# Optimization experiments

Measured on AMD Instinct MI355X. Metric: run time of the kernel, lower is better.

Reference implementation:

```python
import jax, jax.numpy as jnp
import numpy as np

H = 128  # hidden_dim


def _lstm_dir(x, w_ih, w_hh, b, reverse):
    """Single-direction LSTM over x:[B,T,I]. PyTorch gate order (i,f,g,o)."""
    B = x.shape[0]
    gx = jnp.einsum('bti,gi->btg', x, w_ih) + b        # [B,T,4H] input-side gates, one batched GEMM
    gx = jnp.swapaxes(gx, 0, 1)                        # [T,B,4H]
    if reverse:
        gx = gx[::-1]

    def step(carry, g_x):
        h, c = carry
        g = g_x + h @ w_hh.T                           # [B,4H]
        i, f, gg, o = jnp.split(g, 4, axis=-1)
        i = jax.nn.sigmoid(i)
        f = jax.nn.sigmoid(f)
        gg = jnp.tanh(gg)
        o = jax.nn.sigmoid(o)
        c = f * c + i * gg
        h = o * jnp.tanh(c)
        return (h, c), h

    init = (jnp.zeros((B, H), x.dtype), jnp.zeros((B, H), x.dtype))
    (hT, cT), hs = jax.lax.scan(step, init, gx)        # hs:[T,B,H]
    hs = jnp.swapaxes(hs, 0, 1)                        # [B,T,H]
    if reverse:
        hs = hs[:, ::-1]
    return hs, hT, cT


def _bilstm_layer(x, pf, pb):
    hf, hTf, cTf = _lstm_dir(x, *pf, reverse=False)
    hb, hTb, cTb = _lstm_dir(x, *pb, reverse=True)
    return jnp.concatenate([hf, hb], axis=-1), (hTf, cTf), (hTb, cTb)


def setup_inputs() -> dict:
    key = jax.random.key(0)
    ks = jax.random.split(key, 13)
    s = 1.0 / np.sqrt(H)
    B, T, I = 256, 512, 24
    d = {"x": jax.random.normal(ks[0], (B, T, I), jnp.float32)}
    # layer 0 input dim = 24; layer 1 input dim = 2*H = 256
    dims = {"l0f": I, "l0b": I, "l1f": 2 * H, "l1b": 2 * H}
    i = 1
    for tag, din in dims.items():
        d[f"w_ih_{tag}"] = jax.random.uniform(ks[i], (4 * H, din), jnp.float32, -s, s); i += 1
        d[f"w_hh_{tag}"] = jax.random.uniform(ks[i], (4 * H, H), jnp.float32, -s, s); i += 1
        d[f"b_{tag}"] = jax.random.uniform(ks[i], (4 * H,), jnp.float32, -s, s); i += 1
    return d


def reference(x,
              w_ih_l0f, w_hh_l0f, b_l0f, w_ih_l0b, w_hh_l0b, b_l0b,
              w_ih_l1f, w_hh_l1f, b_l1f, w_ih_l1b, w_hh_l1b, b_l1b):
    # Layer 0 (bidirectional)
    y0, (hTf0, cTf0), (hTb0, cTb0) = _bilstm_layer(
        x, (w_ih_l0f, w_hh_l0f, b_l0f), (w_ih_l0b, w_hh_l0b, b_l0b))
    # Inter-layer dropout is identity in eval mode.
    # Layer 1 (bidirectional)
    y1, (hTf1, cTf1), (hTb1, cTb1) = _bilstm_layer(
        y0, (w_ih_l1f, w_hh_l1f, b_l1f), (w_ih_l1b, w_hh_l1b, b_l1b))
    # PyTorch h_n/c_n layout: [num_layers*num_dirs, B, H] ordered l0f,l0b,l1f,l1b
    h_n = jnp.stack([hTf0, hTb0, hTf1, hTb1], axis=0)
    c_n = jnp.stack([cTf0, cTb0, cTf1, cTb1], axis=0)
    return y1, h_n, c_n
```

## Files before the change

kernel.cpp:

```cpp
#include <hip/hip_runtime.h>
#include <hip/hip_bf16.h>
#include <stdint.h>

#define Bn 256
#define Tn 512
#define Hn 128
#define G4 512
#define Mn (Bn*Tn)

typedef __attribute__((ext_vector_type(8))) short s16x8;
typedef __attribute__((ext_vector_type(4))) float f32x4;

__device__ __forceinline__ float b2f(unsigned short u) {
    union { unsigned int i; float f; } v; v.i = ((unsigned int)u) << 16; return v.f;
}
__device__ __forceinline__ unsigned short f2b(float f) {
    union { float f; unsigned int i; } v; v.f = f;
    unsigned int x = v.i;
    unsigned int r = (x + 0x7FFFu + ((x >> 16) & 1u)) >> 16;
    return (unsigned short)r;
}
__device__ __forceinline__ unsigned int pk2(float a, float b) {
    __hip_bfloat162 t = __float22bfloat162_rn(make_float2(a, b));
    union { __hip_bfloat162 v; unsigned int u; } c; c.v = t; return c.u;
}
__device__ __forceinline__ s16x8 cvt8v(const float* p) {
    f32x4 a = *(const f32x4*)p;
    f32x4 b = *(const f32x4*)(p + 4);
    s16x8 r;
    r[0] = (short)f2b(a[0]); r[1] = (short)f2b(a[1]);
    r[2] = (short)f2b(a[2]); r[3] = (short)f2b(a[3]);
    r[4] = (short)f2b(b[0]); r[5] = (short)f2b(b[1]);
    r[6] = (short)f2b(b[2]); r[7] = (short)f2b(b[3]);
    return r;
}
__device__ __forceinline__ float sigm(float x) {
    return __builtin_amdgcn_rcpf(1.f + __expf(-x));
}
__device__ __forceinline__ float tanh_f(float x) {
    return 1.f - 2.f * __builtin_amdgcn_rcpf(1.f + __expf(2.f * x));
}
__device__ __forceinline__ void gload16(const void* gsrc, void* lds) {
    __builtin_amdgcn_global_load_lds(
        (const __attribute__((address_space(1))) unsigned int*)gsrc,
        (__attribute__((address_space(3))) unsigned int*)lds, 16, 0, 0);
}
__device__ __forceinline__ void ldsbar() {
    asm volatile("s_waitcnt lgkmcnt(0)\n\ts_barrier" ::: "memory");
}

__global__ __launch_bounds__(256)
void prep(const float* __restrict__ x,
          const float* __restrict__ w0f, const float* __restrict__ w0b,
          const float* __restrict__ w1f, const float* __restrict__ w1b,
          unsigned short* __restrict__ xb,
          unsigned short* __restrict__ w0bf,
          unsigned short* __restrict__ w1bf)
{
    int tid = blockIdx.x * 256 + threadIdx.x;
    int nthr = gridDim.x * 256;
    for (int idx = tid; idx < Mn * 32; idx += nthr) {
        int row = idx >> 5, col = idx & 31;
        xb[idx] = f2b(col < 24 ? x[row * 24 + col] : 0.f);
    }
    for (int idx = tid; idx < 2 * 512 * 32; idx += nthr) {
        int d = idx >> 14, rem = idx & 16383;
        int n = rem >> 5, col = rem & 31;
        const float* w = d ? w0b : w0f;
        w0bf[idx] = f2b(col < 24 ? w[n * 24 + col] : 0.f);
    }
    for (int idx = tid; idx < 2 * 512 * 256; idx += nthr) {
        int d = idx >> 17, rem = idx & 131071;
        const float* w = d ? w1b : w1f;
        w1bf[idx] = f2b(w[rem]);
    }
}

template<int BK, int KOUT>
__global__ __launch_bounds__(256, 2)
void gemm_tile(const unsigned short* __restrict__ A, int lda,
               const unsigned short* __restrict__ W,
               unsigned short* __restrict__ gx)
{
    constexpr int GR = BK / 8;
    constexpr int SWM = (GR >= 8) ? 7 : (GR - 1);
    constexpr int ASZ = 128 * BK * 2;
    constexpr int GOFF = (BK == 128) ? 0 : 2 * ASZ;
    constexpr int SMEM = 2 * ASZ + ((BK == 128) ? 0 : 4 * 16 * 68 * 4);
    __shared__ char smem[SMEM];
    unsigned short* Atile = (unsigned short*)smem;
    unsigned short* Btile = (unsigned short*)(smem + ASZ);

    const int K = BK * KOUT;
    const int mb = blockIdx.x;
    const int nb = blockIdx.y;
    const int dir = nb >> 2, ncol0 = (nb & 3) * 128;
    const int row0 = mb * 128;
    const unsigned short* Asrc = A + (size_t)row0 * lda;
    const unsigned short* Bsrc = W + (size_t)dir * 512 * K + (size_t)ncol0 * K;
    unsigned short* out = gx + (size_t)dir * Mn * G4;

    const int tid = threadIdx.x;
    const int w = tid >> 6, l = tid & 63;
    const int q = l >> 4, i = l & 15;
    const int wm = w >> 1, wn = w & 1;

    f32x4 acc[4][4];
#pragma unroll
    for (int a = 0; a < 4; ++a)
#pragma unroll
        for (int b = 0; b < 4; ++b) acc[a][b] = f32x4{0.f, 0.f, 0.f, 0.f};

    for (int ko = 0; ko < KOUT; ++ko) {
#pragma unroll
        for (int it = 0; it < (128 * GR) / 256; ++it) {
            int g = it * 256 + tid;
            int row = g / GR, p = g % GR;
            int gi = p ^ (row & SWM);
            gload16(Asrc + (size_t)row * lda + ko * BK + gi * 8,
                    (char*)Atile + g * 16);
        }
#pragma unroll
        for (int it = 0; it < (128 * GR) / 256; ++it) {
            int g = it * 256 + tid;
            int row = g / GR, p = g % GR;
            int gi = p ^ (row & SWM);
            gload16(Bsrc + (size_t)row * K + ko * BK + gi * 8,
                    (char*)Btile + g * 16);
        }
        __syncthreads();
#pragma unroll
        for (int kf = 0; kf < BK / 32; ++kf) {
            s16x8 af[4], bf[4];
#pragma unroll
            for (int mt = 0; mt < 4; ++mt) {
                int ar = wm * 64 + mt * 16 + i;
                int p = (kf * 4 + q) ^ (ar & SWM);
                af[mt] = *(const s16x8*)((char*)Atile + (ar * GR + p) * 16);
            }
#pragma unroll
            for (int nt = 0; nt < 4; ++nt) {
                int br = wn * 64 + nt * 16 + i;
                int p = (kf * 4 + q) ^ (br & SWM);
                bf[nt] = *(const s16x8*)((char*)Btile + (br * GR + p) * 16);
            }
#pragma unroll
            for (int mt = 0; mt < 4; ++mt)
#pragma unroll
                for (int nt = 0; nt < 4; ++nt)
                    acc[mt][nt] = __builtin_amdgcn_mfma_f32_16x16x32_bf16(
                        af[mt], bf[nt], acc[mt][nt], 0, 0, 0);
        }
        __syncthreads();
    }

    float* gbufw = (float*)(smem + GOFF) + w * (16 * 68);
#pragma unroll
    for (int mt = 0; mt < 4; ++mt) {
#pragma unroll
        for (int nt = 0; nt < 4; ++nt)
#pragma unroll
            for (int r = 0; r < 4; ++r)
                gbufw[(q * 4 + r) * 68 + nt * 16 + i] = acc[mt][nt][r];
        __syncthreads();
#pragma unroll
        for (int it2 = 0; it2 < 2; ++it2) {
            int rr = (l >> 3) + it2 * 8;
            int cc = (l & 7) * 8;
            const float* gsrc = gbufw + rr * 68 + cc;
            uint4 pv;
            pv.x = pk2(gsrc[0], gsrc[1]);
            pv.y = pk2(gsrc[2], gsrc[3]);
            pv.z = pk2(gsrc[4], gsrc[5]);
            pv.w = pk2(gsrc[6], gsrc[7]);
            *(uint4*)(out + (size_t)(row0 + wm * 64 + mt * 16 + rr) * G4
                          + ncol0 + wn * 64 + cc) = pv;
        }
        __syncthreads();
    }
}

__global__ __launch_bounds__(256, 1)
void lstm_rec(const unsigned short* __restrict__ gx,
              const float* __restrict__ Whf,
              const float* __restrict__ Whb,
              const float* __restrict__ biasf,
              const float* __restrict__ biasb,
              float* __restrict__ y,
              unsigned short* __restrict__ y0b,
              float* __restrict__ hn,
              float* __restrict__ cn,
              int layer)
{
    const int b0  = blockIdx.x * 2;
    const int dir = blockIdx.y;
    const float* Wh   = dir ? Whb : Whf;
    const float* bias = dir ? biasb : biasf;
    const unsigned short* gxd = gx + (size_t)dir * Mn * G4;

    const int tid = threadIdx.x;
    const int w = tid >> 6, l = tid & 63;
    const int q = l >> 4, i = l & 15;

    __shared__ unsigned short hbuf[16][136];
    __shared__ float Gs[512][2];

    for (int idx = tid; idx < 16 * 136; idx += 256)
        ((unsigned short*)hbuf)[idx] = 0;

    s16x8 wh[8][4];
#pragma unroll
    for (int nt = 0; nt < 8; ++nt) {
        int n = w * 128 + nt * 16 + i;
#pragma unroll
        for (int kf = 0; kf < 4; ++kf)
            wh[nt][kf] = cvt8v(Wh + (size_t)n * Hn + kf * 32 + q * 8);
    }

    const int m = tid >> 7;
    const int j = tid & 127;
    const int b = b0 + m;
    const float bi = bias[j],       bf = bias[128 + j];
    const float bg = bias[256 + j], bo = bias[384 + j];
    float c = 0.f, hlast = 0.f;

    unsigned short bufA[4][8], bufB[4][8];
#pragma unroll
    for (int f = 0; f < 8; ++f) {
        int t = dir ? (Tn - 1 - f) : f;
        const unsigned short* gp = gxd + ((size_t)b * Tn + t) * G4;
        bufA[0][f] = gp[j];
        bufA[1][f] = gp[128 + j];
        bufA[2][f] = gp[256 + j];
        bufA[3][f] = gp[384 + j];
    }

    __syncthreads();

    auto do8 = [&](unsigned short (&useB)[4][8], unsigned short (&ldB)[4][8],
                   int sb) {
#pragma unroll
        for (int f = 0; f < 8; ++f) {
            const int s = sb + f;
            const int t = dir ? (Tn - 1 - s) : s;

            s16x8 ah[4];
#pragma unroll
            for (int kf = 0; kf < 4; ++kf)
                ah[kf] = *(const s16x8*)(&hbuf[i][kf * 32 + q * 8]);
            f32x4 acc[8];
#pragma unroll
            for (int nt = 0; nt < 8; ++nt) {
                acc[nt] = f32x4{0.f, 0.f, 0.f, 0.f};
#pragma unroll
                for (int kf = 0; kf < 4; ++kf)
                    acc[nt] = __builtin_amdgcn_mfma_f32_16x16x32_bf16(
                        ah[kf], wh[nt][kf], acc[nt], 0, 0, 0);
            }
            if (q == 0) {
#pragma unroll
                for (int nt = 0; nt < 8; ++nt) {
                    int n = w * 128 + nt * 16 + i;
                    Gs[n][0] = acc[nt][0];
                    Gs[n][1] = acc[nt][1];
                }
            }
            {
                int sl = (s + 8 < Tn) ? (s + 8) : s;
                int tl = dir ? (Tn - 1 - sl) : sl;
                const unsigned short* gp = gxd + ((size_t)b * Tn + tl) * G4;
                ldB[0][f] = gp[j];
                ldB[1][f] = gp[128 + j];
                ldB[2][f] = gp[256 + j];
                ldB[3][f] = gp[384 + j];
            }
            ldsbar();

            float gi = Gs[j][m]       + b2f(useB[0][f]) + bi;
            float gf = Gs[128 + j][m] + b2f(useB[1][f]) + bf;
            float gg = Gs[256 + j][m] + b2f(useB[2][f]) + bg;
            float go = Gs[384 + j][m] + b2f(useB[3][f]) + bo;
            float iv = sigm(gi), fv = sigm(gf), ov = sigm(go);
            float gv = tanh_f(gg);
            c = fv * c + iv * gv;
            float h = ov * tanh_f(c);
            hlast = h;
            unsigned short hb = f2b(h);
            hbuf[m][j] = hb;
            if (layer == 0)
                y0b[((size_t)b * Tn + t) * 256 + dir * 128 + j] = hb;
            else
                y[((size_t)b * Tn + t) * 256 + dir * 128 + j] = h;

            ldsbar();
        }
    };

    for (int sb = 0; sb < Tn; sb += 16) {
        do8(bufA, bufB, sb);
        do8(bufB, bufA, sb + 8);
    }

    const int slot = layer * 2 + dir;
    hn[((size_t)slot * Bn + b) * Hn + j] = hlast;
    cn[((size_t)slot * Bn + b) * Hn + j] = c;
}

extern "C" void kernel_launch(void* const* d_in, const int* in_sizes, int n_in,
                              void* d_out, int out_size, void* d_ws, size_t ws_size,
                              hipStream_t stream)
{
    const float* x     = (const float*)d_in[0];
    const float* wih0f = (const float*)d_in[1];
    const float* whh0f = (const float*)d_in[2];
    const float* b0f   = (const float*)d_in[3];
    const float* wih0b = (const float*)d_in[4];
    const float* whh0b = (const float*)d_in[5];
    const float* b0b   = (const float*)d_in[6];
    const float* wih1f = (const float*)d_in[7];
    const float* whh1f = (const float*)d_in[8];
    const float* b1f   = (const float*)d_in[9];
    const float* wih1b = (const float*)d_in[10];
    const float* whh1b = (const float*)d_in[11];
    const float* b1b   = (const float*)d_in[12];

    float* y  = (float*)d_out;
    float* hn = y + (size_t)Mn * 256;
    float* cn = hn + (size_t)4 * Bn * Hn;
    unsigned short* gx = (unsigned short*)d_ws;

    unsigned short* scr  = (unsigned short*)d_out;
    unsigned short* y0b  = scr;
    unsigned short* xb   = scr + (size_t)Mn * 256;
    unsigned short* w0bf = xb  + (size_t)Mn * 32;
    unsigned short* w1bf = w0bf + 2 * 512 * 32;

    prep<<<2048, 256, 0, stream>>>(x, wih0f, wih0b, wih1f, wih1b, xb, w0bf, w1bf);

    dim3 gg(1024, 8), gb(256);
    dim3 rg(128, 2), rb(256);

    gemm_tile<32, 1><<<gg, gb, 0, stream>>>(xb, 32, w0bf, gx);
    lstm_rec<<<rg, rb, 0, stream>>>(gx, whh0f, whh0b, b0f, b0b, y, y0b, hn, cn, 0);
    gemm_tile<128, 2><<<gg, gb, 0, stream>>>(y0b, 256, w1bf, gx);
    lstm_rec<<<rg, rb, 0, stream>>>(gx, whh1f, whh1b, b1f, b1b, y, y0b, hn, cn, 1);
}
```

Before: 1.004 ms.

## Process four batch rows per LSTM block using 512 threads and split gate columns

The recurrent LSTM kernel now handles four batch rows per block with 512 threads (8 waves) instead of two rows with 256 threads. The 512 gate columns are split across 8 waves, so each wave holds half as many recurrent-weight fragments and issues half as many MFMAs per step. The gate staging buffer is widened to stride 5 so all four MFMA output rows can be stored. The aim is to halve the grid, cut per-wave MFMA latency on the serial time chain, and reuse each weight load across more batch rows, at the cost of a larger barrier scope per step.

```diff
diff --git a/kernel.cpp b/kernel.cpp
--- a/kernel.cpp
+++ b/kernel.cpp
@@ -180,7 +180,7 @@
     }
 }
 
-__global__ __launch_bounds__(256, 1)
+__global__ __launch_bounds__(512, 1)
 void lstm_rec(const unsigned short* __restrict__ gx,
               const float* __restrict__ Whf,
               const float* __restrict__ Whb,
@@ -192,7 +192,7 @@
               float* __restrict__ cn,
               int layer)
 {
-    const int b0  = blockIdx.x * 2;
+    const int b0  = blockIdx.x * 4;
     const int dir = blockIdx.y;
     const float* Wh   = dir ? Whb : Whf;
     const float* bias = dir ? biasb : biasf;
@@ -203,18 +203,18 @@
     const int q = l >> 4, i = l & 15;
 
     __shared__ unsigned short hbuf[16][136];
-    __shared__ float Gs[512][2];
-
-    for (int idx = tid; idx < 16 * 136; idx += 256)
+    __shared__ float Gs[512 * 5];
+
+    for (int idx = tid; idx < 16 * 136; idx += 512)
         ((unsigned short*)hbuf)[idx] = 0;
 
-    s16x8 wh[8][4];
-#pragma unroll
-    for (int nt = 0; nt < 8; ++nt) {
-        int n = w * 128 + nt * 16 + i;
+    s16x8 wh[4][4];
+#pragma unroll
+    for (int tt = 0; tt < 4; ++tt) {
+        int n = w * 64 + tt * 16 + i;
 #pragma unroll
         for (int kf = 0; kf < 4; ++kf)
-            wh[nt][kf] = cvt8v(Wh + (size_t)n * Hn + kf * 32 + q * 8);
+            wh[tt][kf] = cvt8v(Wh + (size_t)n * Hn + kf * 32 + q * 8);
     }
 
     const int m = tid >> 7;
@@ -237,6 +237,8 @@
 
     __syncthreads();
 
+    const f32x4 zf = f32x4{0.f, 0.f, 0.f, 0.f};
+
     auto do8 = [&](unsigned short (&useB)[4][8], unsigned short (&ldB)[4][8],
                    int sb) {
 #pragma unroll
@@ -248,21 +250,21 @@
 #pragma unroll
             for (int kf = 0; kf < 4; ++kf)
                 ah[kf] = *(const s16x8*)(&hbuf[i][kf * 32 + q * 8]);
-            f32x4 acc[8];
-#pragma unroll
-            for (int nt = 0; nt < 8; ++nt) {
-                acc[nt] = f32x4{0.f, 0.f, 0.f, 0.f};
-#pragma unroll
-                for (int kf = 0; kf < 4; ++kf)
-                    acc[nt] = __builtin_amdgcn_mfma_f32_16x16x32_bf16(
-                        ah[kf], wh[nt][kf], acc[nt], 0, 0, 0);
+            f32x4 acc[4];
+#pragma unroll
+            for (int tt = 0; tt < 4; ++tt) {
+                acc[tt] = __builtin_amdgcn_mfma_f32_16x16x32_bf16(ah[0], wh[tt][0], zf, 0, 0, 0);
+#pragma unroll
+                for (int kf = 1; kf < 4; ++kf)
+                    acc[tt] = __builtin_amdgcn_mfma_f32_16x16x32_bf16(ah[kf], wh[tt][kf], acc[tt], 0, 0, 0);
             }
             if (q == 0) {
 #pragma unroll
-                for (int nt = 0; nt < 8; ++nt) {
-                    int n = w * 128 + nt * 16 + i;
-                    Gs[n][0] = acc[nt][0];
-                    Gs[n][1] = acc[nt][1];
+                for (int tt = 0; tt < 4; ++tt) {
+                    int n = w * 64 + tt * 16 + i;
+#pragma unroll
+                    for (int r = 0; r < 4; ++r)
+                        Gs[n * 5 + r] = acc[tt][r];
                 }
             }
             {
@@ -276,10 +278,10 @@
             }
             ldsbar();
 
-            float gi = Gs[j][m]       + b2f(useB[0][f]) + bi;
-            float gf = Gs[128 + j][m] + b2f(useB[1][f]) + bf;
-            float gg = Gs[256 + j][m] + b2f(useB[2][f]) + bg;
-            float go = Gs[384 + j][m] + b2f(useB[3][f]) + bo;
+            float gi = Gs[j * 5 + m]         + b2f(useB[0][f]) + bi;
+            float gf = Gs[(128 + j) * 5 + m] + b2f(useB[1][f]) + bf;
+            float gg = Gs[(256 + j) * 5 + m] + b2f(useB[2][f]) + bg;
+            float go = Gs[(384 + j) * 5 + m] + b2f(useB[3][f]) + bo;
             float iv = sigm(gi), fv = sigm(gf), ov = sigm(go);
             float gv = tanh_f(gg);
             c = fv * c + iv * gv;
@@ -338,7 +340,7 @@
     prep<<<2048, 256, 0, stream>>>(x, wih0f, wih0b, wih1f, wih1b, xb, w0bf, w1bf);
 
     dim3 gg(1024, 8), gb(256);
-    dim3 rg(128, 2), rb(256);
+    dim3 rg(64, 2), rb(512);
 
     gemm_tile<32, 1><<<gg, gb, 0, stream>>>(xb, 32, w0bf, gx);
     lstm_rec<<<rg, rb, 0, stream>>>(gx, whh0f, whh0b, b0f, b0b, y, y0b, hn, cn, 0);
```

Result: slower. 1.034 ms (+3.0%).
